# Kernel tuning notes

Hardware: AMD Instinct MI355X
Metric: run time of the kernel (lower is better)

The kernel has to match this reference:

```python
import jax, jax.numpy as jnp
import numpy as np

WIN = (2, 2, 8, 8)
NUM_HEADS = 6
DIM = 120
HID = int(DIM * 2.0)
SHAPE = (8, 4, 64, 64, DIM)


def _layernorm(x, w, b, eps=1e-5):
    m = jnp.mean(x, axis=-1, keepdims=True)
    v = jnp.mean((x - m) ** 2, axis=-1, keepdims=True)
    return (x - m) / jnp.sqrt(v + eps) * w + b


def _window_partition(x, win):
    N, D, H, W, C = x.shape
    x = x.reshape(N // win[0], win[0], D // win[1], win[1],
                  H // win[2], win[2], W // win[3], win[3], C)
    x = jnp.transpose(x, (0, 2, 4, 6, 1, 3, 5, 7, 8))
    return x.reshape(-1, win[0] * win[1] * win[2] * win[3], C)


def _window_reverse(wins, win, N, D, H, W):
    x = wins.reshape(N // win[0], D // win[1], H // win[2], W // win[3],
                     win[0], win[1], win[2], win[3], -1)
    x = jnp.transpose(x, (0, 4, 1, 5, 2, 6, 3, 7, 8))
    return x.reshape(N, D, H, W, -1)


def _mha(q, k, v, scale):
    # q,k,v: (B_, h, n, hd) -> (B_, n, h*hd)
    a = jax.nn.softmax(jnp.einsum('bhid,bhjd->bhij', q * scale, k), axis=-1)
    o = jnp.einsum('bhij,bhjd->bhid', a, v)
    B, h, n, hd = o.shape
    return jnp.transpose(o, (0, 2, 1, 3)).reshape(B, n, h * hd)


def _qkv(xw, W, b, heads):
    B, n, C = xw.shape
    qkv = (xw @ W.T + b).reshape(B, n, 3, heads, C // heads)
    qkv = jnp.transpose(qkv, (2, 0, 3, 1, 4))
    return qkv[0], qkv[1], qkv[2]


def _tmsa(x, norm1_w, norm1_b, qkv_self_w, qkv_self_b, qkv_mut_w, qkv_mut_b,
          proj_w, proj_b, norm2_w, norm2_b, fc11_w, fc11_b, fc12_w, fc12_b,
          fc2_w, fc2_b):
    N, D, H, W, C = x.shape
    heads = NUM_HEADS
    scale = (C // heads) ** -0.5
    # --- attention branch (no shift -> no roll, no mask; dims divide window -> no pad) ---
    h = _layernorm(x, norm1_w, norm1_b)
    xw = _window_partition(h, WIN)                       # (B_, n, C)
    q, k, v = _qkv(xw, qkv_self_w, qkv_self_b, heads)
    x_self = _mha(q, k, v, scale)                        # (B_, n, C)
    q, k, v = _qkv(xw, qkv_mut_w, qkv_mut_b, heads)
    n = xw.shape[1]
    q1, q2 = q[:, :, :n // 2], q[:, :, n // 2:]
    k1, k2 = k[:, :, :n // 2], k[:, :, n // 2:]
    v1, v2 = v[:, :, :n // 2], v[:, :, n // 2:]
    x1 = _mha(q2, k1, v1, scale)                         # (B_, n/2, C)
    x2 = _mha(q1, k2, v2, scale)
    x_mut = jnp.concatenate([x1, x2], axis=1)            # (B_, n, C)
    x_out = jnp.concatenate([x_mut, x_self], axis=2)     # (B_, n, 2C)
    attn = x_out @ proj_w.T + proj_b                     # (B_, n, C)
    attn = _window_reverse(attn, WIN, N, D, H, W)
    x = x + attn
    # --- GEGLU MLP branch ---
    h2 = _layernorm(x, norm2_w, norm2_b)
    gate = jax.nn.gelu(h2 @ fc11_w.T + fc11_b, approximate=False)
    hid = gate * (h2 @ fc12_w.T + fc12_b)
    x = x + (hid @ fc2_w.T + fc2_b)
    return x


def setup_inputs() -> dict:
    key = jax.random.key(0)
    ks = jax.random.split(key, 8)
    s = 0.02
    return {
        'x': jax.random.normal(ks[0], SHAPE, dtype=jnp.float32),
        'norm1_w': jnp.ones((DIM,), jnp.float32),
        'norm1_b': jnp.zeros((DIM,), jnp.float32),
        'qkv_self_w': jax.random.normal(ks[1], (3 * DIM, DIM), jnp.float32) * s,
        'qkv_self_b': jnp.zeros((3 * DIM,), jnp.float32),
        'qkv_mut_w': jax.random.normal(ks[2], (3 * DIM, DIM), jnp.float32) * s,
        'qkv_mut_b': jnp.zeros((3 * DIM,), jnp.float32),
        'proj_w': jax.random.normal(ks[3], (DIM, 2 * DIM), jnp.float32) * s,
        'proj_b': jnp.zeros((DIM,), jnp.float32),
        'norm2_w': jnp.ones((DIM,), jnp.float32),
        'norm2_b': jnp.zeros((DIM,), jnp.float32),
        'fc11_w': jax.random.normal(ks[4], (HID, DIM), jnp.float32) * s,
        'fc11_b': jnp.zeros((HID,), jnp.float32),
        'fc12_w': jax.random.normal(ks[5], (HID, DIM), jnp.float32) * s,
        'fc12_b': jnp.zeros((HID,), jnp.float32),
        'fc2_w': jax.random.normal(ks[6], (DIM, HID), jnp.float32) * s,
        'fc2_b': jnp.zeros((DIM,), jnp.float32),
    }


def reference(x, norm1_w, norm1_b, qkv_self_w, qkv_self_b, qkv_mut_w,
              qkv_mut_b, proj_w, proj_b, norm2_w, norm2_b, fc11_w, fc11_b,
              fc12_w, fc12_b, fc2_w, fc2_b):
    return _tmsa(x, norm1_w, norm1_b, qkv_self_w, qkv_self_b, qkv_mut_w,
                 qkv_mut_b, proj_w, proj_b, norm2_w, norm2_b, fc11_w, fc11_b,
                 fc12_w, fc12_b, fc2_w, fc2_b)
```

## Files before the change

kernel.cpp:

```cpp
#include <hip/hip_runtime.h>
#include <hip/hip_bf16.h>
#include <math.h>


typedef __attribute__((ext_vector_type(8))) short bf16x8;
typedef __attribute__((ext_vector_type(4))) float f32x4;

#define SCALE2 (0.22360679774997896f * 1.44269504088896340f)
#define CHROWS 65536
#define QPLANE 7864320u
#define KPAD 136

union B8U { bf16x8 v; uint4 u4; uint2 u2[2]; unsigned u[4]; short s[8]; };

__device__ __forceinline__ short bf16b(float f) {
    __hip_bfloat16 h = __float2bfloat16(f);
    return *reinterpret_cast<short*>(&h);
}
__device__ __forceinline__ float bf2f(short s) {
    return __uint_as_float(((unsigned)(unsigned short)s) << 16);
}
__device__ __forceinline__ unsigned packbf(float a, float b) {
    return (unsigned)(unsigned short)bf16b(a) |
           ((unsigned)(unsigned short)bf16b(b) << 16);
}

__device__ __forceinline__ int rev_row(int r) {
    int w = r >> 8, t = r & 255;
    int w8 = w & 7, h8 = (w >> 3) & 7, d2 = (w >> 6) & 1, n2 = w >> 7;
    int www = t & 7, hh = (t >> 3) & 7, dd = (t >> 6) & 1, nn = t >> 7;
    int n = n2 * 2 + nn, d = d2 * 2 + dd;
    int Hc = h8 * 8 + hh, Wc = w8 * 8 + www;
    return ((n * 4 + d) << 12) + (Hc << 6) + Wc;
}
__device__ __forceinline__ int part_row(int g) {
    int ww = g & 63, hh = (g >> 6) & 63, d = (g >> 12) & 3, n = g >> 14;
    int w = ((n >> 1) * 2 + (d >> 1)) * 64 + ((hh >> 3) << 3) + (ww >> 3);
    int t = (((n & 1) * 2 + (d & 1)) << 6) + ((hh & 7) << 3) + (ww & 7);
    return (w << 8) + t;
}
__device__ __forceinline__ float gelu_exact(float x) {
    return 0.5f * x * (1.0f + erff(x * 0.70710678118654752f));
}

__device__ __forceinline__ bf16x8 load_frag20(const short* row, int quad) {
    B8U r;
    const uint2* p = (const uint2*)(row + quad * 8);
    r.u2[0] = p[0]; r.u2[1] = p[1];
    if (quad == 2) { r.u[2] = 0; r.u[3] = 0; }
    else if (quad == 3) { r.u[0] = r.u[1] = r.u[2] = r.u[3] = 0; }
    return r.v;
}

__device__ __forceinline__ void stage_A(short* As, const short* __restrict__ A,
                                        int bm, int k0, int Astr, int tid) {
#pragma unroll
    for (int i = 0; i < 8; ++i) {
        int c = tid + i * 256;
        if (c < 1920) {
            int row = c / 15, slot = c - row * 15;
            uint4 v = *(const uint4*)(A + (size_t)(bm + row) * Astr + k0 + slot * 8);
            *(uint4*)(As + row * KPAD + slot * 8) = v;
        }
    }
    if (tid < 128) *(uint4*)(As + tid * KPAD + 120) = make_uint4(0u, 0u, 0u, 0u);
}
__device__ __forceinline__ void stage_W(short* Ws, const float* __restrict__ W,
                                        int bn, int k0, int Wstr, int N, int tid) {
#pragma unroll
    for (int i = 0; i < 8; ++i) {
        int c = tid + i * 256;
        if (c < 1920) {
            int row = c / 30, slot = c - row * 30;
            int wr = bn + row; if (wr > N - 1) wr = N - 1;
            f32x4 v = *(const f32x4*)(W + (size_t)wr * Wstr + k0 + slot * 4);
            *(uint2*)(Ws + row * KPAD + slot * 4) = make_uint2(packbf(v.x, v.y),
                                                               packbf(v.z, v.w));
        }
    }
    if (tid < 64) *(uint4*)(Ws + tid * KPAD + 120) = make_uint4(0u, 0u, 0u, 0u);
}

template <bool REMAP>
__global__ __launch_bounds__(256) void ln_kernel(const float* __restrict__ in,
                                                 const float* __restrict__ w,
                                                 const float* __restrict__ b,
                                                 short* __restrict__ out) {
    int row  = blockIdx.x * 4 + (threadIdx.x >> 6);
    int lane = threadIdx.x & 63;
    const float* xr = in + (size_t)row * 120;
    float2 v = make_float2(0.f, 0.f);
    if (lane < 60) v = *(const float2*)(xr + lane * 2);
    float s = v.x + v.y;
#pragma unroll
    for (int off = 32; off; off >>= 1) s += __shfl_down(s, off, 64);
    s = __shfl(s, 0, 64);
    float mean = s * (1.f / 120.f);
    float dx = v.x - mean, dy = v.y - mean;
    float q = (lane < 60) ? (dx * dx + dy * dy) : 0.f;
#pragma unroll
    for (int off = 32; off; off >>= 1) q += __shfl_down(q, off, 64);
    q = __shfl(q, 0, 64);
    float rstd = rsqrtf(q * (1.f / 120.f) + 1e-5f);
    int orow = REMAP ? part_row(row) : row;
    if (lane < 60) {
        float2 wv = *(const float2*)(w + lane * 2);
        float2 bv = *(const float2*)(b + lane * 2);
        unsigned u = packbf(dx * rstd * wv.x + bv.x, dy * rstd * wv.y + bv.y);
        *(unsigned*)(out + (size_t)orow * 120 + lane * 2) = u;
    }
}

template <int MODE, int K, int N>
__global__ __launch_bounds__(256) void mm(const short* __restrict__ A,
                                          const float* __restrict__ W,
                                          const float* __restrict__ bias,
                                          void* __restrict__ outp,
                                          const float* __restrict__ aux,
                                          int m0) {
    __shared__ __align__(16) short As[128 * KPAD];
    __shared__ __align__(16) short Ws[64 * KPAD];
    const int tid = threadIdx.x;
    const int lane = tid & 63, wave = tid >> 6;
    const int quad = lane >> 4, l16 = lane & 15;
    const int bmb = blockIdx.x * 128;
    const int bn  = blockIdx.y * 64;
    const int abase = (wave >> 1) * 64;
    const int wbase = (wave & 1) * 32;

    f32x4 acc[4][2];
#pragma unroll
    for (int i = 0; i < 4; ++i)
#pragma unroll
        for (int j = 0; j < 2; ++j) acc[i][j] = (f32x4){0.f, 0.f, 0.f, 0.f};

    constexpr int PH = K / 120;
#pragma unroll
    for (int p = 0; p < PH; ++p) {
        if (p) __syncthreads();
        stage_A(As, A, bmb, p * 120, K, tid);
        stage_W(Ws, W, bn, p * 120, K, N, tid);
        __syncthreads();
        const short* Ab = As + (abase + l16) * KPAD + quad * 8;
        const short* Wb = Ws + (wbase + l16) * KPAD + quad * 8;
#pragma unroll
        for (int kt = 0; kt < 4; ++kt) {
            bf16x8 b0 = *(const bf16x8*)(Wb + kt * 32);
            bf16x8 b1 = *(const bf16x8*)(Wb + 16 * KPAD + kt * 32);
#pragma unroll
            for (int i = 0; i < 4; ++i) {
                bf16x8 a = *(const bf16x8*)(Ab + i * 16 * KPAD + kt * 32);
                acc[i][0] = __builtin_amdgcn_mfma_f32_16x16x32_bf16(a, b0, acc[i][0], 0, 0, 0);
                acc[i][1] = __builtin_amdgcn_mfma_f32_16x16x32_bf16(a, b1, acc[i][1], 0, 0, 0);
            }
        }
    }

    const int bm = bmb + abase;
#pragma unroll
    for (int j = 0; j < 2; ++j) {
        const int n = bn + wbase + j * 16 + l16;
        if (n >= N) continue;
        const float bs = bias[n];
        int which = 0, head = 0, e = 0;
        if (MODE == 0) { which = n / 120; int hn = n % 120; head = hn / 20; e = hn % 20; }
#pragma unroll
        for (int i = 0; i < 4; ++i) {
#pragma unroll
            for (int r = 0; r < 4; ++r) {
                int m = bm + i * 16 + quad * 4 + r;
                float val = acc[i][j][r] + bs;
                if (MODE == 0) {
                    if (which == 0) val *= SCALE2;
                    int wl = m >> 8, t = m & 255;
                    ((short*)outp)[(size_t)which * QPLANE +
                                   ((size_t)((wl * 6 + head) * 256 + t)) * 20 + e] = bf16b(val);
                } else if (MODE == 1) {
                    int g = rev_row(m0 + m);
                    val += aux[(size_t)g * 120 + n];
                    ((float*)outp)[(size_t)(m0 + m) * 120 + n] = val;
                } else {
                    int g = rev_row(m0 + m);
                    val += aux[(size_t)m * 120 + n];
                    ((float*)outp)[(size_t)g * 120 + n] = val;
                }
            }
        }
    }
}

__global__ __launch_bounds__(256) void mm_mlp(const short* __restrict__ A,
                                              const float* __restrict__ W1,
                                              const float* __restrict__ b1,
                                              const float* __restrict__ W2,
                                              const float* __restrict__ b2,
                                              short* __restrict__ outp) {
    __shared__ __align__(16) short As[128 * KPAD];
    __shared__ __align__(16) short Wa[64 * KPAD];
    __shared__ __align__(16) short Wbs[64 * KPAD];
    const int tid = threadIdx.x;
    const int lane = tid & 63, wave = tid >> 6;
    const int quad = lane >> 4, l16 = lane & 15;
    const int bmb = blockIdx.x * 128;
    const int bn  = blockIdx.y * 64;
    const int abase = (wave >> 1) * 64;
    const int wbase = (wave & 1) * 32;
    const int N = 240;

    f32x4 acc1[4][2], acc2[4][2];
#pragma unroll
    for (int i = 0; i < 4; ++i)
#pragma unroll
        for (int j = 0; j < 2; ++j) {
            acc1[i][j] = (f32x4){0.f, 0.f, 0.f, 0.f};
            acc2[i][j] = (f32x4){0.f, 0.f, 0.f, 0.f};
        }

    stage_A(As, A, bmb, 0, 120, tid);
    stage_W(Wa, W1, bn, 0, 120, N, tid);
    stage_W(Wbs, W2, bn, 0, 120, N, tid);
    __syncthreads();
    const short* Ab  = As  + (abase + l16) * KPAD + quad * 8;
    const short* W1b = Wa  + (wbase + l16) * KPAD + quad * 8;
    const short* W2b = Wbs + (wbase + l16) * KPAD + quad * 8;
#pragma unroll
    for (int kt = 0; kt < 4; ++kt) {
        bf16x8 p0 = *(const bf16x8*)(W1b + kt * 32);
        bf16x8 p1 = *(const bf16x8*)(W1b + 16 * KPAD + kt * 32);
        bf16x8 q0 = *(const bf16x8*)(W2b + kt * 32);
        bf16x8 q1 = *(const bf16x8*)(W2b + 16 * KPAD + kt * 32);
#pragma unroll
        for (int i = 0; i < 4; ++i) {
            bf16x8 a = *(const bf16x8*)(Ab + i * 16 * KPAD + kt * 32);
            acc1[i][0] = __builtin_amdgcn_mfma_f32_16x16x32_bf16(a, p0, acc1[i][0], 0, 0, 0);
            acc1[i][1] = __builtin_amdgcn_mfma_f32_16x16x32_bf16(a, p1, acc1[i][1], 0, 0, 0);
            acc2[i][0] = __builtin_amdgcn_mfma_f32_16x16x32_bf16(a, q0, acc2[i][0], 0, 0, 0);
            acc2[i][1] = __builtin_amdgcn_mfma_f32_16x16x32_bf16(a, q1, acc2[i][1], 0, 0, 0);
        }
    }

    const int bm = bmb + abase;
#pragma unroll
    for (int j = 0; j < 2; ++j) {
        const int n = bn + wbase + j * 16 + l16;
        if (n >= N) continue;
        const float g1 = b1[n], g2 = b2[n];
#pragma unroll
        for (int i = 0; i < 4; ++i) {
#pragma unroll
            for (int r = 0; r < 4; ++r) {
                int m = bm + i * 16 + quad * 4 + r;
                float gv = acc1[i][j][r] + g1;
                float vv = acc2[i][j][r] + g2;
                outp[(size_t)m * 240 + n] = bf16b(gelu_exact(gv) * vv);
            }
        }
    }
}

template <int NK, bool MUT>
__global__ __launch_bounds__(NK) void attn_flash(const short* __restrict__ qkv,
                                                 short* __restrict__ xout) {
    constexpr int NKT = NK / 32;
    constexpr int VSTR2 = NK + 4;
    __shared__ __align__(16) short Kf[NKT * 2 * 48 * 8];
    __shared__ __align__(16) unsigned Vt2[11 * VSTR2];
    const int b = blockIdx.x;
    int wl, hd, half;
    if (MUT) { half = b & 1; hd = (b >> 1) % 6; wl = b / 12; }
    else     { half = 0;     hd = b % 6;        wl = b / 6;  }
    const int tid  = threadIdx.x;
    const int lane = tid & 63, wave = tid >> 6;
    const int quad = lane >> 4, l16 = lane & 15;

    const size_t rb = (size_t)(wl * 6 + hd) * 256;
    const short* qpl = qkv + rb * 20;
    const short* kpl = qkv + (size_t)QPLANE + rb * 20;
    const short* vpl = qkv + 2 * (size_t)QPLANE + rb * 20;
    const int koff = MUT ? half * 128 : 0;
    const int qoff = MUT ? (1 - half) * 128 : 0;

    {
        const uint2* p = (const uint2*)(vpl + (size_t)(koff + tid) * 20);
        unsigned tmp[10];
#pragma unroll
        for (int i = 0; i < 5; ++i) ((uint2*)tmp)[i] = p[i];
#pragma unroll
        for (int i = 0; i < 10; ++i) Vt2[i * VSTR2 + tid] = tmp[i];
        Vt2[10 * VSTR2 + tid] = 0x00003F80u;

        int skt = tid >> 5, sf = (tid >> 4) & 1, sl = tid & 15;
        int srow = koff + skt * 32 + sf * 4 + ((sl >> 2) << 3) + (sl & 3);
        const uint2* kp = (const uint2*)(kpl + (size_t)srow * 20);
        uint2 k0 = kp[0], k1 = kp[1], k2 = kp[2], k3 = kp[3], k4 = kp[4];
        uint4* dst = (uint4*)Kf + ((skt * 2 + sf) * 48 + sl);
        dst[0]  = make_uint4(k0.x, k0.y, k1.x, k1.y);
        dst[16] = make_uint4(k2.x, k2.y, k3.x, k3.y);
        dst[32] = make_uint4(k4.x, k4.y, 0u, 0u);
    }
    __syncthreads();

    const int quadc = quad < 3 ? quad : 2;
    const uint4* kfrag = (const uint4*)Kf + quadc * 16 + l16;
    const unsigned sel = (l16 & 1) ? 0x07060302u : 0x05040100u;
    const unsigned* vbase0 = Vt2 + (l16 >> 1) * VSTR2;
    int r1 = 8 + (l16 >> 1); if (r1 > 10) r1 = 10;
    const unsigned* vbase1 = Vt2 + r1 * VSTR2;
    const f32x4 z4 = {0.f, 0.f, 0.f, 0.f};

#pragma unroll 1
    for (int g = 0; g < 2; ++g) {
        bf16x8 bq0 = load_frag20(qpl + (size_t)(qoff + wave * 64 + (g * 2 + 0) * 16 + l16) * 20, quad);
        bf16x8 bq1 = load_frag20(qpl + (size_t)(qoff + wave * 64 + (g * 2 + 1) * 16 + l16) * 20, quad);

        f32x4 accO[2][2];
        accO[0][0] = z4; accO[0][1] = z4; accO[1][0] = z4; accO[1][1] = z4;

#pragma unroll
        for (int kt = 0; kt < NKT; ++kt) {
            B8U ak0, ak1;
            ak0.u4 = kfrag[(kt * 2 + 0) * 48];
            ak1.u4 = kfrag[(kt * 2 + 1) * 48];
            B8U av0, av1;
            {
                uint4 va = *(const uint4*)(vbase0 + kt * 32 + quad * 8);
                uint4 vb = *(const uint4*)(vbase0 + kt * 32 + quad * 8 + 4);
                av0.u[0] = __builtin_amdgcn_perm(va.y, va.x, sel);
                av0.u[1] = __builtin_amdgcn_perm(va.w, va.z, sel);
                av0.u[2] = __builtin_amdgcn_perm(vb.y, vb.x, sel);
                av0.u[3] = __builtin_amdgcn_perm(vb.w, vb.z, sel);
                uint4 vc = *(const uint4*)(vbase1 + kt * 32 + quad * 8);
                uint4 vd = *(const uint4*)(vbase1 + kt * 32 + quad * 8 + 4);
                av1.u[0] = __builtin_amdgcn_perm(vc.y, vc.x, sel);
                av1.u[1] = __builtin_amdgcn_perm(vc.w, vc.z, sel);
                av1.u[2] = __builtin_amdgcn_perm(vd.y, vd.x, sel);
                av1.u[3] = __builtin_amdgcn_perm(vd.w, vd.z, sel);
            }
#pragma unroll
            for (int t = 0; t < 2; ++t) {
                bf16x8 bqt = t ? bq1 : bq0;
                f32x4 s0 = __builtin_amdgcn_mfma_f32_16x16x32_bf16(ak0.v, bqt, z4, 0, 0, 0);
                f32x4 s1 = __builtin_amdgcn_mfma_f32_16x16x32_bf16(ak1.v, bqt, z4, 0, 0, 0);
                float p0 = __builtin_amdgcn_exp2f(s0[0]), p1 = __builtin_amdgcn_exp2f(s0[1]);
                float p2 = __builtin_amdgcn_exp2f(s0[2]), p3 = __builtin_amdgcn_exp2f(s0[3]);
                float p4 = __builtin_amdgcn_exp2f(s1[0]), p5 = __builtin_amdgcn_exp2f(s1[1]);
                float p6 = __builtin_amdgcn_exp2f(s1[2]), p7 = __builtin_amdgcn_exp2f(s1[3]);
                B8U bp;
                bp.u[0] = packbf(p0, p1);
                bp.u[1] = packbf(p2, p3);
                bp.u[2] = packbf(p4, p5);
                bp.u[3] = packbf(p6, p7);
                accO[t][0] = __builtin_amdgcn_mfma_f32_16x16x32_bf16(av0.v, bp.v, accO[t][0], 0, 0, 0);
                accO[t][1] = __builtin_amdgcn_mfma_f32_16x16x32_bf16(av1.v, bp.v, accO[t][1], 0, 0, 0);
            }
        }

#pragma unroll
        for (int t = 0; t < 2; ++t) {
            int nt = g * 2 + t;
            float l = __shfl(accO[t][1][0], 16 + l16, 64);
            float inv = 1.f / l;
            int tok = (MUT ? half * 128 : 0) + wave * 64 + nt * 16 + l16;
            short* orow = xout + (size_t)(wl * 256 + tok) * 240 + (MUT ? hd * 20 : 120 + hd * 20);
            unsigned lo = packbf(accO[t][0][0] * inv, accO[t][0][1] * inv);
            unsigned hi2 = packbf(accO[t][0][2] * inv, accO[t][0][3] * inv);
            *(uint2*)(orow + quad * 4) = make_uint2(lo, hi2);
            if (quad == 0) {
                unsigned lo2 = packbf(accO[t][1][0] * inv, accO[t][1][1] * inv);
                unsigned hi3 = packbf(accO[t][1][2] * inv, accO[t][1][3] * inv);
                *(uint2*)(orow + 16) = make_uint2(lo2, hi3);
            }
        }
    }
}

extern "C" void kernel_launch(void* const* d_in, const int* in_sizes, int n_in,
                              void* d_out, int out_size, void* d_ws, size_t ws_size,
                              hipStream_t stream) {
    const float* x          = (const float*)d_in[0];
    const float* norm1_w    = (const float*)d_in[1];
    const float* norm1_b    = (const float*)d_in[2];
    const float* qkv_self_w = (const float*)d_in[3];
    const float* qkv_self_b = (const float*)d_in[4];
    const float* qkv_mut_w  = (const float*)d_in[5];
    const float* qkv_mut_b  = (const float*)d_in[6];
    const float* proj_w     = (const float*)d_in[7];
    const float* proj_b     = (const float*)d_in[8];
    const float* norm2_w    = (const float*)d_in[9];
    const float* norm2_b    = (const float*)d_in[10];
    const float* fc11_w     = (const float*)d_in[11];
    const float* fc11_b     = (const float*)d_in[12];
    const float* fc12_w     = (const float*)d_in[13];
    const float* fc12_b     = (const float*)d_in[14];
    const float* fc2_w      = (const float*)d_in[15];
    const float* fc2_b      = (const float*)d_in[16];

    if (ws_size < 110100480u) return;

    char* wsb   = (char*)d_ws;
    short* Hb    = (short*)wsb;
    short* QKVc  = (short*)(wsb + 31457280);
    short* XOUTc = (short*)(wsb + 78643200);
    float* TMP   = (float*)wsb;
    short* H2c   = (short*)(wsb + 62914560);
    short* HIDc  = (short*)(wsb + 78643200);
    float* X2    = (float*)d_out;
    float* out   = (float*)d_out;

    ln_kernel<true><<<32768, 256, 0, stream>>>(x, norm1_w, norm1_b, Hb);

    for (int c = 0; c < 2; ++c) {
        int m0 = c * CHROWS;
        const short* Ac = Hb + (size_t)m0 * 120;
        mm<0, 120, 360><<<dim3(512, 6), 256, 0, stream>>>(Ac, qkv_self_w, qkv_self_b,
                                                          QKVc, nullptr, 0);
        attn_flash<256, false><<<1536, 256, 0, stream>>>(QKVc, XOUTc);
        mm<0, 120, 360><<<dim3(512, 6), 256, 0, stream>>>(Ac, qkv_mut_w, qkv_mut_b,
                                                          QKVc, nullptr, 0);
        attn_flash<128, true><<<3072, 128, 0, stream>>>(QKVc, XOUTc);
        mm<1, 240, 120><<<dim3(512, 2), 256, 0, stream>>>(XOUTc, proj_w, proj_b,
                                                          X2, x, m0);
    }

    hipMemcpyAsync(TMP, d_out, 62914560u, hipMemcpyDeviceToDevice, stream);

    for (int c = 0; c < 2; ++c) {
        int m0 = c * CHROWS;
        ln_kernel<false><<<16384, 256, 0, stream>>>(TMP + (size_t)m0 * 120,
                                                    norm2_w, norm2_b, H2c);
        mm_mlp<<<dim3(512, 4), 256, 0, stream>>>(H2c, fc11_w, fc11_b,
                                                 fc12_w, fc12_b, HIDc);
        mm<4, 240, 120><<<dim3(512, 2), 256, 0, stream>>>(HIDc, fc2_w, fc2_b,
                                                          out, TMP + (size_t)m0 * 120, m0);
    }
}
```

Measured before the change: 650.7 us.

## Store GEMM operands in LDS in MFMA fragment order and reuse one weight buffer

The shared-memory staging for the linear-layer GEMMs now writes A and W tiles in per-lane MFMA fragment order, so each wave reads a contiguous uint4 per lane rather than padded row-major rows. The aim is fewer LDS bank conflicts and simpler addressing on fragment loads. The MLP kernel now stages its two weight matrices one after the other into a single buffer, adding a sync in between, to cut LDS use and possibly raise occupancy. The cost is an extra barrier and the two weight loads are serialized rather than overlapped.

```diff
diff --git a/kernel.cpp b/kernel.cpp
--- a/kernel.cpp
+++ b/kernel.cpp
@@ -9,7 +9,6 @@
 #define SCALE2 (0.22360679774997896f * 1.44269504088896340f)
 #define CHROWS 65536
 #define QPLANE 7864320u
-#define KPAD 136
 
 union B8U { bf16x8 v; uint4 u4; uint2 u2[2]; unsigned u[4]; short s[8]; };
 
@@ -52,33 +51,33 @@
     return r.v;
 }
 
-__device__ __forceinline__ void stage_A(short* As, const short* __restrict__ A,
-                                        int bm, int k0, int Astr, int tid) {
+__device__ __forceinline__ void stageA_frag(uint4* Af, const short* __restrict__ A,
+                                            int bm, int k0, int Astr, int tid) {
 #pragma unroll
     for (int i = 0; i < 8; ++i) {
-        int c = tid + i * 256;
-        if (c < 1920) {
-            int row = c / 15, slot = c - row * 15;
-            uint4 v = *(const uint4*)(A + (size_t)(bm + row) * Astr + k0 + slot * 8);
-            *(uint4*)(As + row * KPAD + slot * 8) = v;
-        }
-    }
-    if (tid < 128) *(uint4*)(As + tid * KPAD + 120) = make_uint4(0u, 0u, 0u, 0u);
-}
-__device__ __forceinline__ void stage_W(short* Ws, const float* __restrict__ W,
-                                        int bn, int k0, int Wstr, int N, int tid) {
-#pragma unroll
-    for (int i = 0; i < 8; ++i) {
-        int c = tid + i * 256;
-        if (c < 1920) {
-            int row = c / 30, slot = c - row * 30;
-            int wr = bn + row; if (wr > N - 1) wr = N - 1;
-            f32x4 v = *(const f32x4*)(W + (size_t)wr * Wstr + k0 + slot * 4);
-            *(uint2*)(Ws + row * KPAD + slot * 4) = make_uint2(packbf(v.x, v.y),
-                                                               packbf(v.z, v.w));
-        }
-    }
-    if (tid < 64) *(uint4*)(Ws + tid * KPAD + 120) = make_uint4(0u, 0u, 0u, 0u);
+        int c = i * 256 + tid;
+        int row = c >> 4, q = c & 15;
+        uint4 v = make_uint4(0u, 0u, 0u, 0u);
+        if (q < 15) v = *(const uint4*)(A + (size_t)(bm + row) * Astr + k0 + q * 8);
+        Af[((row >> 4) * 4 + (q >> 2)) * 64 + (q & 3) * 16 + (row & 15)] = v;
+    }
+}
+__device__ __forceinline__ void stageW_frag(uint4* Wf, const float* __restrict__ W,
+                                            int bn, int k0, int Wstr, int N, int tid) {
+#pragma unroll
+    for (int i = 0; i < 4; ++i) {
+        int c = i * 256 + tid;
+        int row = c >> 4, q = c & 15;
+        int wr = bn + row; if (wr > N - 1) wr = N - 1;
+        uint4 d = make_uint4(0u, 0u, 0u, 0u);
+        if (q < 15) {
+            f32x4 w0 = *(const f32x4*)(W + (size_t)wr * Wstr + k0 + q * 8);
+            f32x4 w1 = *(const f32x4*)(W + (size_t)wr * Wstr + k0 + q * 8 + 4);
+            d = make_uint4(packbf(w0.x, w0.y), packbf(w0.z, w0.w),
+                           packbf(w1.x, w1.y), packbf(w1.z, w1.w));
+        }
+        Wf[((row >> 4) * 4 + (q >> 2)) * 64 + (q & 3) * 16 + (row & 15)] = d;
+    }
 }
 
 template <bool REMAP>
@@ -118,15 +117,15 @@
                                           void* __restrict__ outp,
                                           const float* __restrict__ aux,
                                           int m0) {
-    __shared__ __align__(16) short As[128 * KPAD];
-    __shared__ __align__(16) short Ws[64 * KPAD];
+    __shared__ uint4 Af[2048];
+    __shared__ uint4 Wf[1024];
     const int tid = threadIdx.x;
     const int lane = tid & 63, wave = tid >> 6;
     const int quad = lane >> 4, l16 = lane & 15;
     const int bmb = blockIdx.x * 128;
     const int bn  = blockIdx.y * 64;
-    const int abase = (wave >> 1) * 64;
-    const int wbase = (wave & 1) * 32;
+    const int atile = (wave >> 1) * 4;
+    const int wtile = (wave & 1) * 2;
 
     f32x4 acc[4][2];
 #pragma unroll
@@ -138,28 +137,27 @@
 #pragma unroll
     for (int p = 0; p < PH; ++p) {
         if (p) __syncthreads();
-        stage_A(As, A, bmb, p * 120, K, tid);
-        stage_W(Ws, W, bn, p * 120, K, N, tid);
+        stageA_frag(Af, A, bmb, p * 120, K, tid);
+        stageW_frag(Wf, W, bn, p * 120, K, N, tid);
         __syncthreads();
-        const short* Ab = As + (abase + l16) * KPAD + quad * 8;
-        const short* Wb = Ws + (wbase + l16) * KPAD + quad * 8;
 #pragma unroll
         for (int kt = 0; kt < 4; ++kt) {
-            bf16x8 b0 = *(const bf16x8*)(Wb + kt * 32);
-            bf16x8 b1 = *(const bf16x8*)(Wb + 16 * KPAD + kt * 32);
+            B8U b0, b1;
+            b0.u4 = Wf[((wtile + 0) * 4 + kt) * 64 + lane];
+            b1.u4 = Wf[((wtile + 1) * 4 + kt) * 64 + lane];
 #pragma unroll
             for (int i = 0; i < 4; ++i) {
-                bf16x8 a = *(const bf16x8*)(Ab + i * 16 * KPAD + kt * 32);
-                acc[i][0] = __builtin_amdgcn_mfma_f32_16x16x32_bf16(a, b0, acc[i][0], 0, 0, 0);
-                acc[i][1] = __builtin_amdgcn_mfma_f32_16x16x32_bf16(a, b1, acc[i][1], 0, 0, 0);
-            }
-        }
-    }
-
-    const int bm = bmb + abase;
+                B8U a; a.u4 = Af[((atile + i) * 4 + kt) * 64 + lane];
+                acc[i][0] = __builtin_amdgcn_mfma_f32_16x16x32_bf16(a.v, b0.v, acc[i][0], 0, 0, 0);
+                acc[i][1] = __builtin_amdgcn_mfma_f32_16x16x32_bf16(a.v, b1.v, acc[i][1], 0, 0, 0);
+            }
+        }
+    }
+
+    const int bm = bmb + atile * 16;
 #pragma unroll
     for (int j = 0; j < 2; ++j) {
-        const int n = bn + wbase + j * 16 + l16;
+        const int n = bn + wtile * 16 + j * 16 + l16;
         if (n >= N) continue;
         const float bs = bias[n];
         int which = 0, head = 0, e = 0;
@@ -195,16 +193,15 @@
                                               const float* __restrict__ W2,
                                               const float* __restrict__ b2,
                                               short* __restrict__ outp) {
-    __shared__ __align__(16) short As[128 * KPAD];
-    __shared__ __align__(16) short Wa[64 * KPAD];
-    __shared__ __align__(16) short Wbs[64 * KPAD];
+    __shared__ uint4 Af[2048];
+    __shared__ uint4 Wf[1024];
     const int tid = threadIdx.x;
     const int lane = tid & 63, wave = tid >> 6;
     const int quad = lane >> 4, l16 = lane & 15;
     const int bmb = blockIdx.x * 128;
     const int bn  = blockIdx.y * 64;
-    const int abase = (wave >> 1) * 64;
-    const int wbase = (wave & 1) * 32;
+    const int atile = (wave >> 1) * 4;
+    const int wtile = (wave & 1) * 2;
     const int N = 240;
 
     f32x4 acc1[4][2], acc2[4][2];
@@ -216,33 +213,41 @@
             acc2[i][j] = (f32x4){0.f, 0.f, 0.f, 0.f};
         }
 
-    stage_A(As, A, bmb, 0, 120, tid);
-    stage_W(Wa, W1, bn, 0, 120, N, tid);
-    stage_W(Wbs, W2, bn, 0, 120, N, tid);
+    stageA_frag(Af, A, bmb, 0, 120, tid);
+    stageW_frag(Wf, W1, bn, 0, 120, N, tid);
     __syncthreads();
-    const short* Ab  = As  + (abase + l16) * KPAD + quad * 8;
-    const short* W1b = Wa  + (wbase + l16) * KPAD + quad * 8;
-    const short* W2b = Wbs + (wbase + l16) * KPAD + quad * 8;
 #pragma unroll
     for (int kt = 0; kt < 4; ++kt) {
-        bf16x8 p0 = *(const bf16x8*)(W1b + kt * 32);
-        bf16x8 p1 = *(const bf16x8*)(W1b + 16 * KPAD + kt * 32);
-        bf16x8 q0 = *(const bf16x8*)(W2b + kt * 32);
-        bf16x8 q1 = *(const bf16x8*)(W2b + 16 * KPAD + kt * 32);
+        B8U b0, b1;
+        b0.u4 = Wf[((wtile + 0) * 4 + kt) * 64 + lane];
+        b1.u4 = Wf[((wtile + 1) * 4 + kt) * 64 + lane];
 #pragma unroll
         for (int i = 0; i < 4; ++i) {
-            bf16x8 a = *(const bf16x8*)(Ab + i * 16 * KPAD + kt * 32);
-            acc1[i][0] = __builtin_amdgcn_mfma_f32_16x16x32_bf16(a, p0, acc1[i][0], 0, 0, 0);
-            acc1[i][1] = __builtin_amdgcn_mfma_f32_16x16x32_bf16(a, p1, acc1[i][1], 0, 0, 0);
-            acc2[i][0] = __builtin_amdgcn_mfma_f32_16x16x32_bf16(a, q0, acc2[i][0], 0, 0, 0);
-            acc2[i][1] = __builtin_amdgcn_mfma_f32_16x16x32_bf16(a, q1, acc2[i][1], 0, 0, 0);
-        }
-    }
-
-    const int bm = bmb + abase;
+            B8U a; a.u4 = Af[((atile + i) * 4 + kt) * 64 + lane];
+            acc1[i][0] = __builtin_amdgcn_mfma_f32_16x16x32_bf16(a.v, b0.v, acc1[i][0], 0, 0, 0);
+            acc1[i][1] = __builtin_amdgcn_mfma_f32_16x16x32_bf16(a.v, b1.v, acc1[i][1], 0, 0, 0);
+        }
+    }
+    __syncthreads();
+    stageW_frag(Wf, W2, bn, 0, 120, N, tid);
+    __syncthreads();
+#pragma unroll
+    for (int kt = 0; kt < 4; ++kt) {
+        B8U b0, b1;
+        b0.u4 = Wf[((wtile + 0) * 4 + kt) * 64 + lane];
+        b1.u4 = Wf[((wtile + 1) * 4 + kt) * 64 + lane];
+#pragma unroll
+        for (int i = 0; i < 4; ++i) {
+            B8U a; a.u4 = Af[((atile + i) * 4 + kt) * 64 + lane];
+            acc2[i][0] = __builtin_amdgcn_mfma_f32_16x16x32_bf16(a.v, b0.v, acc2[i][0], 0, 0, 0);
+            acc2[i][1] = __builtin_amdgcn_mfma_f32_16x16x32_bf16(a.v, b1.v, acc2[i][1], 0, 0, 0);
+        }
+    }
+
+    const int bm = bmb + atile * 16;
 #pragma unroll
     for (int j = 0; j < 2; ++j) {
-        const int n = bn + wbase + j * 16 + l16;
+        const int n = bn + wtile * 16 + j * 16 + l16;
         if (n >= N) continue;
         const float g1 = b1[n], g2 = b2[n];
 #pragma unroll
```

Measured after the change: 623.2 us. 4.2% less time.
